# Kernel optimization log

Hardware: AMD Instinct MI355X
Metric: run time of the kernel (lower is better)

The kernel has to match this reference:

```python
import jax, jax.numpy as jnp
import numpy as np

E = 512       # embed_dim
H = 8         # num_heads
DH = E // H   # head dim
F = 2048      # dim_feedforward
KS = 33       # NATTEN kernel_size (dilation=1)
NCLS = 1
B = 2
L = 4096      # local tokens (total seq = L + NCLS)
EPS = 1e-5


def layernorm(x, g, b):
    mu = jnp.mean(x, axis=-1, keepdims=True)
    var = jnp.mean(jnp.square(x - mu), axis=-1, keepdims=True)
    return (x - mu) * jax.lax.rsqrt(var + EPS) * g + b


def natten_1d(x, qkv_w, qkv_b, proj_w, proj_b):
    # Neighborhood attention 1D, dilation=1, non-causal, no rel-pos bias.
    b, l, e = x.shape
    qkv = x @ qkv_w.T + qkv_b                       # [b, l, 3E]
    q, k, v = jnp.split(qkv, 3, axis=-1)
    q = q.reshape(b, l, H, DH) * (DH ** -0.5)
    k = k.reshape(b, l, H, DH)
    v = v.reshape(b, l, H, DH)
    # NATTEN window: centered, shifted at edges to keep exactly KS in-bounds neighbors
    starts = jnp.clip(jnp.arange(l) - KS // 2, 0, l - KS)   # [l]
    idx = starts[:, None] + jnp.arange(KS)                  # [l, KS]
    kn = k[:, idx]                                          # [b, l, KS, H, DH]
    vn = v[:, idx]                                          # [b, l, KS, H, DH]
    attn = jnp.einsum('blhd,blkhd->bhlk', q, kn)
    attn = jax.nn.softmax(attn, axis=-1)
    out = jnp.einsum('bhlk,blkhd->blhd', attn, vn).reshape(b, l, e)
    return out @ proj_w.T + proj_b


def global_mha(q_in, kv_in, in_w, in_b, out_w, out_b):
    # torch nn.MultiheadAttention, batch_first, no masks
    bq, lq, e = q_in.shape
    lk = kv_in.shape[1]
    wq, wk, wv = jnp.split(in_w, 3, axis=0)
    bqp, bkp, bvp = jnp.split(in_b, 3, axis=0)
    q = (q_in @ wq.T + bqp).reshape(bq, lq, H, DH) * (DH ** -0.5)
    k = (kv_in @ wk.T + bkp).reshape(bq, lk, H, DH)
    v = (kv_in @ wv.T + bvp).reshape(bq, lk, H, DH)
    attn = jax.nn.softmax(jnp.einsum('bqhd,bkhd->bhqk', q, k), axis=-1)
    out = jnp.einsum('bhqk,bkhd->bqhd', attn, v).reshape(bq, lq, e)
    return out @ out_w.T + out_b


def setup_inputs() -> dict:
    key = jax.random.key(0)
    ks = jax.random.split(key, 16)
    s = 0.02
    return {
        'x': jax.random.normal(ks[0], (B, L + NCLS, E), jnp.float32),
        'ln1_g': jnp.ones((E,), jnp.float32),
        'ln1_b': jnp.zeros((E,), jnp.float32),
        'qkv_w': jax.random.normal(ks[1], (3 * E, E), jnp.float32) * s,
        'qkv_b': jnp.zeros((3 * E,), jnp.float32),
        'na_proj_w': jax.random.normal(ks[2], (E, E), jnp.float32) * s,
        'na_proj_b': jnp.zeros((E,), jnp.float32),
        'in_proj_w': jax.random.normal(ks[3], (3 * E, E), jnp.float32) * s,
        'in_proj_b': jnp.zeros((3 * E,), jnp.float32),
        'out_w': jax.random.normal(ks[4], (E, E), jnp.float32) * s,
        'out_b': jnp.zeros((E,), jnp.float32),
        'ln2_g': jnp.ones((E,), jnp.float32),
        'ln2_b': jnp.zeros((E,), jnp.float32),
        'fc1_w': jax.random.normal(ks[5], (F, E), jnp.float32) * s,
        'fc1_b': jnp.zeros((F,), jnp.float32),
        'fc2_w': jax.random.normal(ks[6], (E, F), jnp.float32) * s,
        'fc2_b': jnp.zeros((E,), jnp.float32),
    }


def reference(x, ln1_g, ln1_b, qkv_w, qkv_b, na_proj_w, na_proj_b,
              in_proj_w, in_proj_b, out_w, out_b, ln2_g, ln2_b,
              fc1_w, fc1_b, fc2_w, fc2_b):
    res = x
    xn = layernorm(x, ln1_g, ln1_b)
    x_local = natten_1d(xn[:, :-NCLS, :], qkv_w, qkv_b, na_proj_w, na_proj_b)
    tmp_key = jnp.concatenate([x_local, xn[:, -NCLS:, :]], axis=1)
    x_cls = global_mha(xn[:, -NCLS:, :], tmp_key, in_proj_w, in_proj_b, out_w, out_b)
    x = res + jnp.concatenate([x_local, x_cls], axis=1)
    res = x
    xn = layernorm(x, ln2_g, ln2_b)
    h = jax.nn.silu(xn @ fc1_w.T + fc1_b)
    return res + (h @ fc2_w.T + fc2_b)
```

## Files before the change

### kernel.cpp

```cpp
#include <hip/hip_runtime.h>
#include <hip/hip_bf16.h>
#include <cstdint>
#include <cstddef>

#define E    512
#define H    8
#define DHD  64
#define FDIM 2048
#define KS   33
#define BB   2
#define LL   4096
#define LP1  4097
#define NTOK 8194
#define NLOC 8192

typedef unsigned short ushort_t;
typedef __bf16 bf16x8_t __attribute__((ext_vector_type(8)));
typedef float  f32x4_t  __attribute__((ext_vector_type(4)));

__device__ __forceinline__ float b2f(unsigned short h) {
  union { unsigned int u; float f; } un; un.u = ((unsigned int)h) << 16; return un.f;
}
__device__ __forceinline__ unsigned short f2b(float f) {
  union { float f; unsigned int u; } un; un.f = f;
  unsigned int u = un.u;
  return (unsigned short)((u + 0x7FFFu + ((u >> 16) & 1u)) >> 16);
}

__device__ __forceinline__ void gload16(const ushort_t* g, ushort_t* l) {
  __builtin_amdgcn_global_load_lds(
      (const __attribute__((address_space(1))) void*)g,
      (__attribute__((address_space(3))) void*)l,
      16, 0, 0);
}

#define BM 128
#define BN 128
#define BK 32

template<int ACT, int OUTF, int ADDRES, int INRM, int OUTRM>
__global__ __launch_bounds__(256) void gemm_bt(
    const ushort_t* __restrict__ A, const ushort_t* __restrict__ W,
    const float* __restrict__ bias, float* __restrict__ outF,
    ushort_t* __restrict__ outB, const float* __restrict__ res,
    int M, int N, int K)
{
  __shared__ ushort_t Alds[BM * BK];
  __shared__ ushort_t Blds[BN * BK];
  const int t    = threadIdx.x;
  const int lane = t & 63;
  const int w    = t >> 6;
  const int wr   = w >> 1, wc = w & 1;
  const int bmBase = blockIdx.x * BM;
  const int bnBase = blockIdx.y * BN;

  f32x4_t zero = {0.f, 0.f, 0.f, 0.f};
  f32x4_t acc[4][4];
  #pragma unroll
  for (int m = 0; m < 4; ++m)
    #pragma unroll
    for (int n = 0; n < 4; ++n) acc[m][n] = zero;

  int r0 = bmBase + (t >> 2);
  int r1 = r0 + 64;
  if (INRM) { r0 += r0 >> 12; r1 += r1 >> 12; }
  else      { if (r0 >= M) r0 = M - 1; if (r1 >= M) r1 = M - 1; }
  const int ako = (t & 3) * 8;
  const int n0  = bnBase + (t >> 2);
  const int n1  = n0 + 64;

  const int frow = lane & 15;
  const int fk   = (lane >> 4) * 8;

  for (int k0 = 0; k0 < K; k0 += BK) {
    gload16(A + (size_t)r0 * K + k0 + ako, &Alds[(size_t)t * 8]);
    gload16(A + (size_t)r1 * K + k0 + ako, &Alds[(size_t)(256 + t) * 8]);
    gload16(W + (size_t)n0 * K + k0 + ako, &Blds[(size_t)t * 8]);
    gload16(W + (size_t)n1 * K + k0 + ako, &Blds[(size_t)(256 + t) * 8]);
    __syncthreads();
    bf16x8_t af[4], bfr[4];
    #pragma unroll
    for (int m = 0; m < 4; ++m)
      af[m] = *reinterpret_cast<const bf16x8_t*>(&Alds[(wr * 64 + m * 16 + frow) * BK + fk]);
    #pragma unroll
    for (int n = 0; n < 4; ++n)
      bfr[n] = *reinterpret_cast<const bf16x8_t*>(&Blds[(wc * 64 + n * 16 + frow) * BK + fk]);
    #pragma unroll
    for (int m = 0; m < 4; ++m)
      #pragma unroll
      for (int n = 0; n < 4; ++n)
        acc[m][n] = __builtin_amdgcn_mfma_f32_16x16x32_bf16(af[m], bfr[n], acc[m][n], 0, 0, 0);
    __syncthreads();
  }

  const int rbase = (lane >> 4) * 4;
  const int cbase = lane & 15;
  #pragma unroll
  for (int m = 0; m < 4; ++m) {
    #pragma unroll
    for (int r = 0; r < 4; ++r) {
      int gr = bmBase + wr * 64 + m * 16 + rbase + r;
      if (gr < M) {
        int orow = OUTRM ? gr + (gr >> 12) : gr;
        #pragma unroll
        for (int n = 0; n < 4; ++n) {
          int gc = bnBase + wc * 64 + n * 16 + cbase;
          float v = acc[m][n][r] + bias[gc];
          if (ACT == 1) v = v / (1.f + __expf(-v));
          if (ADDRES) v += res[(size_t)gr * N + gc];
          if (OUTF) outF[(size_t)orow * N + gc] = v;
          else      outB[(size_t)orow * N + gc] = f2b(v);
        }
      }
    }
  }
}

__global__ __launch_bounds__(256) void ln_fused1(
    const float* __restrict__ x, const float* __restrict__ g,
    const float* __restrict__ be, ushort_t* __restrict__ xn,
    ushort_t* __restrict__ tmpk)
{
  __shared__ float sh[4];
  const int row = blockIdx.x;
  const int t = threadIdx.x;
  const float* xr = x + (size_t)row * E;
  float v0 = xr[t], v1 = xr[t + 256];
  float sum = v0 + v1;
  #pragma unroll
  for (int o = 32; o; o >>= 1) sum += __shfl_xor(sum, o);
  if ((t & 63) == 0) sh[t >> 6] = sum;
  __syncthreads();
  float mean = (sh[0] + sh[1] + sh[2] + sh[3]) * (1.f / E);
  __syncthreads();
  float d0 = v0 - mean, d1 = v1 - mean;
  float vs = d0 * d0 + d1 * d1;
  #pragma unroll
  for (int o = 32; o; o >>= 1) vs += __shfl_xor(vs, o);
  if ((t & 63) == 0) sh[t >> 6] = vs;
  __syncthreads();
  float var = (sh[0] + sh[1] + sh[2] + sh[3]) * (1.f / E);
  float rstd = rsqrtf(var + 1e-5f);
  unsigned short o0 = f2b(d0 * rstd * g[t] + be[t]);
  unsigned short o1 = f2b(d1 * rstd * g[t + 256] + be[t + 256]);
  xn[(size_t)row * E + t] = o0;
  xn[(size_t)row * E + t + 256] = o1;
  if ((row % LP1) == LL) {
    tmpk[(size_t)row * E + t] = o0;
    tmpk[(size_t)row * E + t + 256] = o1;
  }
}

__global__ __launch_bounds__(256) void resid_ln2(
    const float* __restrict__ x, const ushort_t* __restrict__ tmpk,
    const float* __restrict__ xcls, const float* __restrict__ g,
    const float* __restrict__ be, float* __restrict__ xa,
    ushort_t* __restrict__ xn2)
{
  __shared__ float sh[4];
  const int row = blockIdx.x;
  const int b = row / LP1, l = row % LP1;
  const int t = threadIdx.x;
  float a0, a1;
  if (l < LL) { a0 = b2f(tmpk[(size_t)row * E + t]); a1 = b2f(tmpk[(size_t)row * E + t + 256]); }
  else        { a0 = xcls[b * E + t];                a1 = xcls[b * E + t + 256]; }
  float v0 = x[(size_t)row * E + t] + a0;
  float v1 = x[(size_t)row * E + t + 256] + a1;
  xa[(size_t)row * E + t] = v0;
  xa[(size_t)row * E + t + 256] = v1;
  float sum = v0 + v1;
  #pragma unroll
  for (int o = 32; o; o >>= 1) sum += __shfl_xor(sum, o);
  if ((t & 63) == 0) sh[t >> 6] = sum;
  __syncthreads();
  float mean = (sh[0] + sh[1] + sh[2] + sh[3]) * (1.f / E);
  __syncthreads();
  float d0 = v0 - mean, d1 = v1 - mean;
  float vs = d0 * d0 + d1 * d1;
  #pragma unroll
  for (int o = 32; o; o >>= 1) vs += __shfl_xor(vs, o);
  if ((t & 63) == 0) sh[t >> 6] = vs;
  __syncthreads();
  float var = (sh[0] + sh[1] + sh[2] + sh[3]) * (1.f / E);
  float rstd = rsqrtf(var + 1e-5f);
  xn2[(size_t)row * E + t]       = f2b(d0 * rstd * g[t] + be[t]);
  xn2[(size_t)row * E + t + 256] = f2b(d1 * rstd * g[t + 256] + be[t + 256]);
}

__global__ __launch_bounds__(256) void natten_mfma(
    const ushort_t* __restrict__ qkv, ushort_t* __restrict__ out)
{
  __shared__ ushort_t KP[4][64 * 64];
  __shared__ ushort_t VT[4][64 * 72];
  const int w    = threadIdx.x >> 6;
  const int lane = threadIdx.x & 63;
  const int task = blockIdx.x * 4 + w;
  const int h  = task & 7;
  const int qb = (task >> 3) & 127;
  const int b  = task >> 10;
  const int l0 = qb * 32;
  const int kb = l0 - 16;
  const ushort_t* base = qkv + (size_t)b * LL * (3 * E);
  ushort_t* Klds = KP[w];
  ushort_t* Vt   = VT[w];

  {
    const int rsub = lane >> 3;
    const int d0   = (lane & 7) * 8;
    #pragma unroll
    for (int i = 0; i < 8; ++i) {
      int row = i * 8 + rsub;
      int gl = kb + row; gl = gl < 0 ? 0 : (gl > LL - 1 ? LL - 1 : gl);
      bf16x8_t kv = *reinterpret_cast<const bf16x8_t*>(
          base + (size_t)gl * (3 * E) + E + h * 64 + d0);
      int ba = (row * 128 + d0 * 2) ^ ((row & 7) << 4);
      *reinterpret_cast<bf16x8_t*>((char*)Klds + ba) = kv;
    }
  }
  {
    const int a  = lane & 7;
    const int c8 = lane >> 3;
    unsigned int* Vt32 = (unsigned int*)Vt;
    #pragma unroll
    for (int i = 0; i < 4; ++i) {
      int rp = i * 8 + c8;
      int g0 = kb + rp * 2;     g0 = g0 < 0 ? 0 : (g0 > LL - 1 ? LL - 1 : g0);
      int g1 = kb + rp * 2 + 1; g1 = g1 < 0 ? 0 : (g1 > LL - 1 ? LL - 1 : g1);
      const ushort_t* v0 = base + (size_t)g0 * (3 * E) + 2 * E + h * 64 + a * 8;
      const ushort_t* v1 = base + (size_t)g1 * (3 * E) + 2 * E + h * 64 + a * 8;
      ushort4 x0 = *(const ushort4*)v0,       x1 = *(const ushort4*)v1;
      ushort4 y0 = *(const ushort4*)(v0 + 4), y1 = *(const ushort4*)(v1 + 4);
      int d = a * 8;
      Vt32[(d + 0) * 36 + rp] = (unsigned)x0.x | ((unsigned)x1.x << 16);
      Vt32[(d + 1) * 36 + rp] = (unsigned)x0.y | ((unsigned)x1.y << 16);
      Vt32[(d + 2) * 36 + rp] = (unsigned)x0.z | ((unsigned)x1.z << 16);
      Vt32[(d + 3) * 36 + rp] = (unsigned)x0.w | ((unsigned)x1.w << 16);
      Vt32[(d + 4) * 36 + rp] = (unsigned)y0.x | ((unsigned)y1.x << 16);
      Vt32[(d + 5) * 36 + rp] = (unsigned)y0.y | ((unsigned)y1.y << 16);
      Vt32[(d + 6) * 36 + rp] = (unsigned)y0.z | ((unsigned)y1.z << 16);
      Vt32[(d + 7) * 36 + rp] = (unsigned)y0.w | ((unsigned)y1.w << 16);
    }
  }

  const int p = lane & 15, g = lane >> 4;
  bf16x8_t qf[2][2];
  #pragma unroll
  for (int mt = 0; mt < 2; ++mt)
    #pragma unroll
    for (int ks = 0; ks < 2; ++ks)
      qf[mt][ks] = *reinterpret_cast<const bf16x8_t*>(
          base + (size_t)(l0 + mt * 16 + p) * (3 * E) + h * 64 + ks * 32 + g * 8);

  f32x4_t zero = {0.f, 0.f, 0.f, 0.f};
  f32x4_t accS[2][4];
  #pragma unroll
  for (int mt = 0; mt < 2; ++mt)
    #pragma unroll
    for (int nt = 0; nt < 4; ++nt) accS[mt][nt] = zero;
  #pragma unroll
  for (int ks = 0; ks < 2; ++ks) {
    bf16x8_t kf[4];
    #pragma unroll
    for (int nt = 0; nt < 4; ++nt) {
      int row = nt * 16 + p;
      int ba = (row * 128 + (ks * 32 + g * 8) * 2) ^ ((row & 7) << 4);
      kf[nt] = *reinterpret_cast<const bf16x8_t*>((char*)Klds + ba);
    }
    #pragma unroll
    for (int mt = 0; mt < 2; ++mt)
      #pragma unroll
      for (int nt = 0; nt < 4; ++nt)
        accS[mt][nt] = __builtin_amdgcn_mfma_f32_16x16x32_bf16(qf[mt][ks], kf[nt], accS[mt][nt], 0, 0, 0);
  }

  ushort_t* Plds = Klds;
  #pragma unroll
  for (int mt = 0; mt < 2; ++mt) {
    #pragma unroll
    for (int r = 0; r < 4; ++r) {
      int lq = l0 + mt * 16 + g * 4 + r;
      int st = lq - 16; st = st < 0 ? 0 : (st > LL - KS ? LL - KS : st);
      int clo = st - kb, chi = clo + 32;
      float sv[4];
      float mx = -1e30f;
      #pragma unroll
      for (int nt = 0; nt < 4; ++nt) {
        int c = nt * 16 + p;
        float s = accS[mt][nt][r] * 0.125f;
        s = (c >= clo && c <= chi) ? s : -1e30f;
        sv[nt] = s;
        mx = fmaxf(mx, s);
      }
      mx = fmaxf(mx, __shfl_xor(mx, 1));
      mx = fmaxf(mx, __shfl_xor(mx, 2));
      mx = fmaxf(mx, __shfl_xor(mx, 4));
      mx = fmaxf(mx, __shfl_xor(mx, 8));
      float sum = 0.f;
      #pragma unroll
      for (int nt = 0; nt < 4; ++nt) { float e = __expf(sv[nt] - mx); sv[nt] = e; sum += e; }
      sum += __shfl_xor(sum, 1);
      sum += __shfl_xor(sum, 2);
      sum += __shfl_xor(sum, 4);
      sum += __shfl_xor(sum, 8);
      float inv = 1.f / sum;
      int q = mt * 16 + g * 4 + r;
      #pragma unroll
      for (int nt = 0; nt < 4; ++nt)
        Plds[q * 72 + nt * 16 + p] = f2b(sv[nt] * inv);
    }
  }

  f32x4_t accO[2][4];
  #pragma unroll
  for (int mt = 0; mt < 2; ++mt)
    #pragma unroll
    for (int nt = 0; nt < 4; ++nt) accO[mt][nt] = zero;
  #pragma unroll
  for (int ks = 0; ks < 2; ++ks) {
    bf16x8_t pf[2], vf[4];
    #pragma unroll
    for (int mt = 0; mt < 2; ++mt)
      pf[mt] = *reinterpret_cast<const bf16x8_t*>(
          (char*)Plds + (mt * 16 + p) * 144 + (ks * 32 + g * 8) * 2);
    #pragma unroll
    for (int nt = 0; nt < 4; ++nt)
      vf[nt] = *reinterpret_cast<const bf16x8_t*>(
          (char*)Vt + (nt * 16 + p) * 144 + (ks * 32 + g * 8) * 2);
    #pragma unroll
    for (int mt = 0; mt < 2; ++mt)
      #pragma unroll
      for (int nt = 0; nt < 4; ++nt)
        accO[mt][nt] = __builtin_amdgcn_mfma_f32_16x16x32_bf16(pf[mt], vf[nt], accO[mt][nt], 0, 0, 0);
  }

  #pragma unroll
  for (int mt = 0; mt < 2; ++mt) {
    #pragma unroll
    for (int r = 0; r < 4; ++r) {
      int lq = l0 + mt * 16 + g * 4 + r;
      ushort_t* orow = out + ((size_t)(b * LL) + lq) * E + h * 64;
      #pragma unroll
      for (int nt = 0; nt < 4; ++nt)
        orow[nt * 16 + p] = f2b(accO[mt][nt][r]);
    }
  }
}

__global__ __launch_bounds__(256) void qcls_kernel(
    const ushort_t* __restrict__ xn, const float* __restrict__ inw,
    const float* __restrict__ inb, float* __restrict__ qcls)
{
  int i = blockIdx.x * 256 + threadIdx.x;
  int b = i >> 9, d = i & 511;
  const ushort_t* xr = xn + ((size_t)b * LP1 + LL) * E;
  const float* wr = inw + (size_t)d * E;
  float s = 0.f;
  for (int e = 0; e < E; e += 4) {
    ushort4 xv = *reinterpret_cast<const ushort4*>(xr + e);
    s += b2f(xv.x) * wr[e] + b2f(xv.y) * wr[e + 1] + b2f(xv.z) * wr[e + 2] + b2f(xv.w) * wr[e + 3];
  }
  qcls[i] = (s + inb[d]) * 0.125f;
}

__global__ __launch_bounds__(256) void gscore_kernel(
    const float* __restrict__ qcls, const ushort_t* __restrict__ kv,
    float* __restrict__ sc)
{
  const int wav = blockIdx.x * 4 + (threadIdx.x >> 6);
  if (wav >= BB * LP1) return;
  const int lane = threadIdx.x & 63;
  const int b = wav / LP1, j = wav % LP1;
  const ushort_t* kr = kv + (size_t)wav * 1024 + lane * 8;
  const float* q = qcls + b * E + lane * 8;
  ushort4 ka = *reinterpret_cast<const ushort4*>(kr);
  ushort4 kb4 = *reinterpret_cast<const ushort4*>(kr + 4);
  float s = b2f(ka.x) * q[0] + b2f(ka.y) * q[1] + b2f(ka.z) * q[2] + b2f(ka.w) * q[3]
          + b2f(kb4.x) * q[4] + b2f(kb4.y) * q[5] + b2f(kb4.z) * q[6] + b2f(kb4.w) * q[7];
  s += __shfl_xor(s, 1); s += __shfl_xor(s, 2); s += __shfl_xor(s, 4);
  if ((lane & 7) == 0) sc[((size_t)(b * 8) + (lane >> 3)) * LP1 + j] = s;
}

__global__ __launch_bounds__(256) void gsoftmax_kernel(float* __restrict__ sc)
{
  float* row = sc + (size_t)blockIdx.x * LP1;
  __shared__ float sh[4];
  const int t = threadIdx.x;
  float m = -1e30f;
  for (int i = t; i < LP1; i += 256) m = fmaxf(m, row[i]);
  #pragma unroll
  for (int o = 32; o; o >>= 1) m = fmaxf(m, __shfl_xor(m, o));
  if ((t & 63) == 0) sh[t >> 6] = m;
  __syncthreads();
  m = fmaxf(fmaxf(sh[0], sh[1]), fmaxf(sh[2], sh[3]));
  __syncthreads();
  float s = 0.f;
  for (int i = t; i < LP1; i += 256) { float e = __expf(row[i] - m); row[i] = e; s += e; }
  #pragma unroll
  for (int o = 32; o; o >>= 1) s += __shfl_xor(s, o);
  if ((t & 63) == 0) sh[t >> 6] = s;
  __syncthreads();
  float inv = 1.f / (sh[0] + sh[1] + sh[2] + sh[3]);
  for (int i = t; i < LP1; i += 256) row[i] *= inv;
}

__global__ __launch_bounds__(256) void gpv_kernel(
    const float* __restrict__ sc, const ushort_t* __restrict__ kv,
    float* __restrict__ parts)
{
  __shared__ float red[4][64];
  const int bh = blockIdx.y;
  const int b = bh >> 3, h = bh & 7;
  const int c = blockIdx.x;
  const int lane = threadIdx.x & 63, s4 = threadIdx.x >> 6;
  const int j0 = c * 512;
  const int jend = (j0 + 512 < LP1) ? j0 + 512 : LP1;
  const float* prow = sc + (size_t)bh * LP1;
  const ushort_t* vbase = kv + (size_t)b * LP1 * 1024 + 512 + h * 64 + lane;
  float acc = 0.f;
  for (int j = j0 + s4; j < jend; j += 4)
    acc += prow[j] * b2f(vbase[(size_t)j * 1024]);
  red[s4][lane] = acc;
  __syncthreads();
  if (s4 == 0)
    parts[((size_t)c * 16 + bh) * 64 + lane] = red[0][lane] + red[1][lane] + red[2][lane] + red[3][lane];
}

__global__ void gpv_reduce(const float* __restrict__ parts, float* __restrict__ oc)
{
  int i = blockIdx.x * 256 + threadIdx.x;
  if (i < BB * E) {
    float s = 0.f;
    #pragma unroll
    for (int c = 0; c < 9; ++c) s += parts[c * 1024 + i];
    oc[i] = s;
  }
}

__global__ __launch_bounds__(256) void xcls_kernel(
    const float* __restrict__ oc, const float* __restrict__ ow,
    const float* __restrict__ ob, float* __restrict__ xc)
{
  int i = blockIdx.x * 256 + threadIdx.x;
  if (i >= BB * E) return;
  int b = i >> 9, n = i & 511;
  const float* o = oc + b * E;
  const float* wr = ow + (size_t)n * E;
  float s = ob[n];
  for (int m = 0; m < E; ++m) s += o[m] * wr[m];
  xc[i] = s;
}

__global__ void cvt_all(
    const float* __restrict__ s0, ushort_t* __restrict__ d0, int n0,
    const float* __restrict__ s1, ushort_t* __restrict__ d1, int n1,
    const float* __restrict__ s2, ushort_t* __restrict__ d2, int n2,
    const float* __restrict__ s3, ushort_t* __restrict__ d3, int n3,
    const float* __restrict__ s4, ushort_t* __restrict__ d4, int n4)
{
  int i = (blockIdx.x * 256 + threadIdx.x) * 4;
  const float* s; ushort_t* d;
  if (i < n0)                { s = s0; d = d0; }
  else if ((i -= n0) < n1)   { s = s1; d = d1; }
  else if ((i -= n1) < n2)   { s = s2; d = d2; }
  else if ((i -= n2) < n3)   { s = s3; d = d3; }
  else if ((i -= n3) < n4)   { s = s4; d = d4; }
  else return;
  float4 v = *reinterpret_cast<const float4*>(s + i);
  ushort4 o;
  o.x = f2b(v.x); o.y = f2b(v.y); o.z = f2b(v.z); o.w = f2b(v.w);
  *reinterpret_cast<ushort4*>(d + i) = o;
}

extern "C" void kernel_launch(void* const* d_in, const int* in_sizes, int n_in,
                              void* d_out, int out_size, void* d_ws, size_t ws_size,
                              hipStream_t stream)
{
  const float* x      = (const float*)d_in[0];
  const float* ln1_g  = (const float*)d_in[1];
  const float* ln1_b  = (const float*)d_in[2];
  const float* qkv_w  = (const float*)d_in[3];
  const float* qkv_b  = (const float*)d_in[4];
  const float* na_w   = (const float*)d_in[5];
  const float* na_b   = (const float*)d_in[6];
  const float* in_w   = (const float*)d_in[7];
  const float* in_b   = (const float*)d_in[8];
  const float* out_w  = (const float*)d_in[9];
  const float* out_b  = (const float*)d_in[10];
  const float* ln2_g  = (const float*)d_in[11];
  const float* ln2_b  = (const float*)d_in[12];
  const float* fc1_w  = (const float*)d_in[13];
  const float* fc1_b  = (const float*)d_in[14];
  const float* fc2_w  = (const float*)d_in[15];
  const float* fc2_b  = (const float*)d_in[16];
  float* out = (float*)d_out;

  char* pws = (char*)d_ws;
  size_t off = 0;
  auto alloc = [&](size_t bytes) {
    void* r = pws + off; off = (off + bytes + 255) & ~(size_t)255; return r;
  };
  ushort_t* w_qkv = (ushort_t*)alloc((size_t)3 * E * E * 2);
  ushort_t* w_na  = (ushort_t*)alloc((size_t)E * E * 2);
  ushort_t* w_in  = (ushort_t*)alloc((size_t)3 * E * E * 2);
  ushort_t* w_fc1 = (ushort_t*)alloc((size_t)FDIM * E * 2);
  ushort_t* w_fc2 = (ushort_t*)alloc((size_t)E * FDIM * 2);
  ushort_t* xn1   = (ushort_t*)alloc((size_t)NTOK * E * 2);
  char*     bigR  = (char*)alloc((size_t)NTOK * FDIM * 2);
  ushort_t* qkvb  = (ushort_t*)bigR;
  ushort_t* natt  = (ushort_t*)(bigR + (size_t)NLOC * 3 * E * 2);
  ushort_t* kvg   = (ushort_t*)bigR;
  ushort_t* hbuf  = (ushort_t*)bigR;
  ushort_t* tmpk  = (ushort_t*)alloc((size_t)NTOK * E * 2);
  float*    sc    = (float*)alloc((size_t)BB * H * LP1 * 4);
  float*    qcls  = (float*)alloc(1024 * 4);
  float*    parts = (float*)alloc(9 * 16 * 64 * 4);
  float*    oc    = (float*)alloc(1024 * 4);
  float*    xcls  = (float*)alloc(1024 * 4);
  float*    xa    = (float*)alloc((size_t)NTOK * E * 4);
  ushort_t* xn2   = xn1;

  cvt_all<<<3840, 256, 0, stream>>>(
      qkv_w, w_qkv, 3 * E * E,
      na_w,  w_na,  E * E,
      in_w,  w_in,  3 * E * E,
      fc1_w, w_fc1, FDIM * E,
      fc2_w, w_fc2, E * FDIM);

  ln_fused1<<<NTOK, 256, 0, stream>>>(x, ln1_g, ln1_b, xn1, tmpk);
  qcls_kernel<<<4, 256, 0, stream>>>(xn1, in_w, in_b, qcls);
  gemm_bt<0,0,0,1,0><<<dim3(NLOC / BM, 3 * E / BN), 256, 0, stream>>>(
      xn1, w_qkv, qkv_b, nullptr, qkvb, nullptr, NLOC, 3 * E, E);
  natten_mfma<<<512, 256, 0, stream>>>(qkvb, natt);
  gemm_bt<0,0,0,0,1><<<dim3(NLOC / BM, E / BN), 256, 0, stream>>>(
      natt, w_na, na_b, nullptr, tmpk, nullptr, NLOC, E, E);
  gemm_bt<0,0,0,0,0><<<dim3((NTOK + BM - 1) / BM, 1024 / BN), 256, 0, stream>>>(
      tmpk, w_in + (size_t)E * E, in_b + E, nullptr, kvg, nullptr, NTOK, 1024, E);
  gscore_kernel<<<(BB * LP1 + 3) / 4, 256, 0, stream>>>(qcls, kvg, sc);
  gsoftmax_kernel<<<BB * H, 256, 0, stream>>>(sc);
  gpv_kernel<<<dim3(9, BB * H), 256, 0, stream>>>(sc, kvg, parts);
  gpv_reduce<<<4, 256, 0, stream>>>(parts, oc);
  xcls_kernel<<<4, 256, 0, stream>>>(oc, out_w, out_b, xcls);
  resid_ln2<<<NTOK, 256, 0, stream>>>(x, tmpk, xcls, ln2_g, ln2_b, xa, xn2);
  gemm_bt<1,0,0,0,0><<<dim3((NTOK + BM - 1) / BM, FDIM / BN), 256, 0, stream>>>(
      xn2, w_fc1, fc1_b, nullptr, hbuf, nullptr, NTOK, FDIM, E);
  gemm_bt<0,1,1,0,0><<<dim3((NTOK + BM - 1) / BM, E / BN), 256, 0, stream>>>(
      hbuf, w_fc2, fc2_b, out, nullptr, xa, NTOK, E, FDIM);
}
```

Baseline: 290.5 us.

## Use BK=64 swizzled LDS tiles and split-K fc2 GEMM with reduce kernel

The GEMM now loads K-tiles of 64 with an XOR-swizzled LDS layout to avoid bank conflicts and halve the number of barriers per K. The N tile is now a template parameter. The fc2 GEMM (K=2048) uses BN=64 with a two-way split-K into separate float buffers, followed by an elementwise reduce that adds the bias and residual, so that more blocks are available to fill the CUs. The cost is extra global traffic for the partial sums and one more kernel launch.

Measured after the change: 287.5 us. No clear change (-1.0%).

```diff
diff --git a/kernel.cpp b/kernel.cpp
--- a/kernel.cpp
+++ b/kernel.cpp
@@ -35,66 +35,85 @@
 }
 
 #define BM 128
-#define BN 128
-#define BK 32
-
-template<int ACT, int OUTF, int ADDRES, int INRM, int OUTRM>
+
+template<int BNT, int ACT, int OUTF, int ADDRES, int INRM, int OUTRM, int PARTIAL>
 __global__ __launch_bounds__(256) void gemm_bt(
     const ushort_t* __restrict__ A, const ushort_t* __restrict__ W,
     const float* __restrict__ bias, float* __restrict__ outF,
     ushort_t* __restrict__ outB, const float* __restrict__ res,
-    int M, int N, int K)
-{
-  __shared__ ushort_t Alds[BM * BK];
-  __shared__ ushort_t Blds[BN * BK];
+    int M, int N, int K, int klen)
+{
+  constexpr int NFRAG = BNT / 32;
+  __shared__ ushort_t Alds[BM * 64];
+  __shared__ ushort_t Blds[BNT * 64];
   const int t    = threadIdx.x;
   const int lane = t & 63;
   const int w    = t >> 6;
   const int wr   = w >> 1, wc = w & 1;
   const int bmBase = blockIdx.x * BM;
-  const int bnBase = blockIdx.y * BN;
+  const int bnBase = blockIdx.y * BNT;
+  const int z    = blockIdx.z;
+  const int kbeg = z * klen;
 
   f32x4_t zero = {0.f, 0.f, 0.f, 0.f};
-  f32x4_t acc[4][4];
+  f32x4_t acc[4][NFRAG];
   #pragma unroll
   for (int m = 0; m < 4; ++m)
     #pragma unroll
-    for (int n = 0; n < 4; ++n) acc[m][n] = zero;
-
-  int r0 = bmBase + (t >> 2);
-  int r1 = r0 + 64;
-  if (INRM) { r0 += r0 >> 12; r1 += r1 >> 12; }
-  else      { if (r0 >= M) r0 = M - 1; if (r1 >= M) r1 = M - 1; }
-  const int ako = (t & 3) * 8;
-  const int n0  = bnBase + (t >> 2);
-  const int n1  = n0 + 64;
+    for (int n = 0; n < NFRAG; ++n) acc[m][n] = zero;
+
+  const int srow = t >> 3;
+  const int jsw8 = ((t & 7) ^ (srow & 7)) * 8;
+  int arow[4];
+  #pragma unroll
+  for (int r = 0; r < 4; ++r) {
+    int rr = bmBase + r * 32 + srow;
+    if (INRM) rr += rr >> 12;
+    else if (rr >= M) rr = M - 1;
+    arow[r] = rr;
+  }
+  int brow[NFRAG];
+  #pragma unroll
+  for (int r = 0; r < NFRAG; ++r) brow[r] = bnBase + r * 32 + srow;
 
   const int frow = lane & 15;
-  const int fk   = (lane >> 4) * 8;
-
-  for (int k0 = 0; k0 < K; k0 += BK) {
-    gload16(A + (size_t)r0 * K + k0 + ako, &Alds[(size_t)t * 8]);
-    gload16(A + (size_t)r1 * K + k0 + ako, &Alds[(size_t)(256 + t) * 8]);
-    gload16(W + (size_t)n0 * K + k0 + ako, &Blds[(size_t)t * 8]);
-    gload16(W + (size_t)n1 * K + k0 + ako, &Blds[(size_t)(256 + t) * 8]);
+  const int g    = lane >> 4;
+
+  for (int k0 = kbeg; k0 < kbeg + klen; k0 += 64) {
+    #pragma unroll
+    for (int r = 0; r < 4; ++r)
+      gload16(A + (size_t)arow[r] * K + k0 + jsw8, &Alds[(size_t)(r * 256 + t) * 8]);
+    #pragma unroll
+    for (int r = 0; r < NFRAG; ++r)
+      gload16(W + (size_t)brow[r] * K + k0 + jsw8, &Blds[(size_t)(r * 256 + t) * 8]);
     __syncthreads();
-    bf16x8_t af[4], bfr[4];
-    #pragma unroll
-    for (int m = 0; m < 4; ++m)
-      af[m] = *reinterpret_cast<const bf16x8_t*>(&Alds[(wr * 64 + m * 16 + frow) * BK + fk]);
-    #pragma unroll
-    for (int n = 0; n < 4; ++n)
-      bfr[n] = *reinterpret_cast<const bf16x8_t*>(&Blds[(wc * 64 + n * 16 + frow) * BK + fk]);
-    #pragma unroll
-    for (int m = 0; m < 4; ++m)
-      #pragma unroll
-      for (int n = 0; n < 4; ++n)
-        acc[m][n] = __builtin_amdgcn_mfma_f32_16x16x32_bf16(af[m], bfr[n], acc[m][n], 0, 0, 0);
+    #pragma unroll
+    for (int kk2 = 0; kk2 < 2; ++kk2) {
+      bf16x8_t af[4], bfv[NFRAG];
+      const int kosw = ((kk2 * 4 + g) ^ (frow & 7)) << 4;
+      #pragma unroll
+      for (int m = 0; m < 4; ++m) {
+        int row = wr * 64 + m * 16 + frow;
+        af[m] = *reinterpret_cast<const bf16x8_t*>((char*)Alds + row * 128 + kosw);
+      }
+      #pragma unroll
+      for (int n = 0; n < NFRAG; ++n) {
+        int row = wc * (BNT / 2) + n * 16 + frow;
+        bfv[n] = *reinterpret_cast<const bf16x8_t*>((char*)Blds + row * 128 + kosw);
+      }
+      #pragma unroll
+      for (int m = 0; m < 4; ++m)
+        #pragma unroll
+        for (int n = 0; n < NFRAG; ++n)
+          acc[m][n] = __builtin_amdgcn_mfma_f32_16x16x32_bf16(af[m], bfv[n], acc[m][n], 0, 0, 0);
+    }
     __syncthreads();
   }
 
-  const int rbase = (lane >> 4) * 4;
-  const int cbase = lane & 15;
+  const int rbase = g * 4;
+  const int cbase = frow;
+  float* po = nullptr;
+  if (PARTIAL) po = (z == 0) ? outF : (float*)outB;
   #pragma unroll
   for (int m = 0; m < 4; ++m) {
     #pragma unroll
@@ -103,17 +122,38 @@
       if (gr < M) {
         int orow = OUTRM ? gr + (gr >> 12) : gr;
         #pragma unroll
-        for (int n = 0; n < 4; ++n) {
-          int gc = bnBase + wc * 64 + n * 16 + cbase;
-          float v = acc[m][n][r] + bias[gc];
-          if (ACT == 1) v = v / (1.f + __expf(-v));
-          if (ADDRES) v += res[(size_t)gr * N + gc];
-          if (OUTF) outF[(size_t)orow * N + gc] = v;
-          else      outB[(size_t)orow * N + gc] = f2b(v);
+        for (int n = 0; n < NFRAG; ++n) {
+          int gc = bnBase + wc * (BNT / 2) + n * 16 + cbase;
+          float v = acc[m][n][r];
+          if (PARTIAL) {
+            po[(size_t)orow * N + gc] = v;
+          } else {
+            v += bias[gc];
+            if (ACT == 1) v = v / (1.f + __expf(-v));
+            if (ADDRES) v += res[(size_t)gr * N + gc];
+            if (OUTF) outF[(size_t)orow * N + gc] = v;
+            else      outB[(size_t)orow * N + gc] = f2b(v);
+          }
         }
       }
     }
   }
+}
+
+__global__ __launch_bounds__(256) void fc2_reduce(
+    float* __restrict__ out, const float* __restrict__ p0,
+    const float* __restrict__ bias, const float* __restrict__ xa)
+{
+  size_t i = (size_t)blockIdx.x * 256 + threadIdx.x;
+  float4 o = reinterpret_cast<const float4*>(out)[i];
+  float4 a = reinterpret_cast<const float4*>(p0)[i];
+  float4 x = reinterpret_cast<const float4*>(xa)[i];
+  float4 bcol = reinterpret_cast<const float4*>(bias)[i & 127];
+  o.x += a.x + x.x + bcol.x;
+  o.y += a.y + x.y + bcol.y;
+  o.z += a.z + x.z + bcol.z;
+  o.w += a.w + x.w + bcol.w;
+  reinterpret_cast<float4*>(out)[i] = o;
 }
 
 __global__ __launch_bounds__(256) void ln_fused1(
@@ -518,6 +558,10 @@
   float*    xcls  = (float*)alloc(1024 * 4);
   float*    xa    = (float*)alloc((size_t)NTOK * E * 4);
   ushort_t* xn2   = xn1;
+  size_t off_before_s0 = off;
+  float*    s0    = (float*)alloc((size_t)NTOK * E * 4);
+  const bool can_split = (off <= ws_size);
+  if (!can_split) off = off_before_s0;
 
   cvt_all<<<3840, 256, 0, stream>>>(
       qkv_w, w_qkv, 3 * E * E,
@@ -528,21 +572,27 @@
 
   ln_fused1<<<NTOK, 256, 0, stream>>>(x, ln1_g, ln1_b, xn1, tmpk);
   qcls_kernel<<<4, 256, 0, stream>>>(xn1, in_w, in_b, qcls);
-  gemm_bt<0,0,0,1,0><<<dim3(NLOC / BM, 3 * E / BN), 256, 0, stream>>>(
-      xn1, w_qkv, qkv_b, nullptr, qkvb, nullptr, NLOC, 3 * E, E);
+  gemm_bt<128,0,0,0,1,0,0><<<dim3(NLOC / BM, 3 * E / 128), 256, 0, stream>>>(
+      xn1, w_qkv, qkv_b, nullptr, qkvb, nullptr, NLOC, 3 * E, E, E);
   natten_mfma<<<512, 256, 0, stream>>>(qkvb, natt);
-  gemm_bt<0,0,0,0,1><<<dim3(NLOC / BM, E / BN), 256, 0, stream>>>(
-      natt, w_na, na_b, nullptr, tmpk, nullptr, NLOC, E, E);
-  gemm_bt<0,0,0,0,0><<<dim3((NTOK + BM - 1) / BM, 1024 / BN), 256, 0, stream>>>(
-      tmpk, w_in + (size_t)E * E, in_b + E, nullptr, kvg, nullptr, NTOK, 1024, E);
+  gemm_bt<128,0,0,0,0,1,0><<<dim3(NLOC / BM, E / 128), 256, 0, stream>>>(
+      natt, w_na, na_b, nullptr, tmpk, nullptr, NLOC, E, E, E);
+  gemm_bt<128,0,0,0,0,0,0><<<dim3((NTOK + BM - 1) / BM, 1024 / 128), 256, 0, stream>>>(
+      tmpk, w_in + (size_t)E * E, in_b + E, nullptr, kvg, nullptr, NTOK, 1024, E, E);
   gscore_kernel<<<(BB * LP1 + 3) / 4, 256, 0, stream>>>(qcls, kvg, sc);
   gsoftmax_kernel<<<BB * H, 256, 0, stream>>>(sc);
   gpv_kernel<<<dim3(9, BB * H), 256, 0, stream>>>(sc, kvg, parts);
   gpv_reduce<<<4, 256, 0, stream>>>(parts, oc);
   xcls_kernel<<<4, 256, 0, stream>>>(oc, out_w, out_b, xcls);
   resid_ln2<<<NTOK, 256, 0, stream>>>(x, tmpk, xcls, ln2_g, ln2_b, xa, xn2);
-  gemm_bt<1,0,0,0,0><<<dim3((NTOK + BM - 1) / BM, FDIM / BN), 256, 0, stream>>>(
-      xn2, w_fc1, fc1_b, nullptr, hbuf, nullptr, NTOK, FDIM, E);
-  gemm_bt<0,1,1,0,0><<<dim3((NTOK + BM - 1) / BM, E / BN), 256, 0, stream>>>(
-      hbuf, w_fc2, fc2_b, out, nullptr, xa, NTOK, E, FDIM);
-}
+  gemm_bt<128,1,0,0,0,0,0><<<dim3((NTOK + BM - 1) / BM, FDIM / 128), 256, 0, stream>>>(
+      xn2, w_fc1, fc1_b, nullptr, hbuf, nullptr, NTOK, FDIM, E, E);
+  if (can_split) {
+    gemm_bt<64,0,0,0,0,0,1><<<dim3((NTOK + BM - 1) / BM, E / 64, 2), 256, 0, stream>>>(
+        hbuf, w_fc2, fc2_b, s0, (ushort_t*)out, nullptr, NTOK, E, FDIM, FDIM / 2);
+    fc2_reduce<<<(NTOK * E / 4) / 256, 256, 0, stream>>>(out, s0, fc2_b, xa);
+  } else {
+    gemm_bt<64,0,1,1,0,0,0><<<dim3((NTOK + BM - 1) / BM, E / 64), 256, 0, stream>>>(
+        hbuf, w_fc2, fc2_b, out, nullptr, xa, NTOK, E, FDIM, FDIM);
+  }
+}
```
